# Performance work log

Measured on AMD Instinct MI355X. Metric: run time of the kernel, lower is better.

The kernel has to match this reference:

```python
import jax, jax.numpy as jnp
import numpy as np

NUM_HEADS = 16
QKV_FEATURES = 2048
HEAD_DIM = QKV_FEATURES // NUM_HEADS
THETA = 10000.0


def compute_freqs_cis(dim, length, start_pos=0, theta=THETA, dtype=jnp.float32):
    freqs = 1.0 / theta ** (jnp.arange(0, dim, 2, dtype=jnp.float32) / dim)
    t = jnp.arange(length, dtype=jnp.float32) + start_pos
    freqs = jnp.outer(t, freqs)  # (L, dim//2)
    return jnp.sin(freqs).astype(dtype), jnp.cos(freqs).astype(dtype)


def apply_rotary_emb(x, sin, cos):
    # x: (B, L, H, D); sin/cos: (L, D//2); interleaved-pair rotation
    x1 = x[..., 0::2]
    x2 = x[..., 1::2]
    sin = sin[None, :, None, :]
    cos = cos[None, :, None, :]
    y1 = x1 * cos - x2 * sin
    y2 = x1 * sin + x2 * cos
    return jnp.stack([y1, y2], axis=-1).reshape(x.shape)


def setup_inputs() -> dict:
    key = jax.random.key(0)
    ks = jax.random.split(key, 6)
    B, L, E = 2, 2048, 2048
    s_in = 1.0 / np.sqrt(E)
    s_out = 1.0 / np.sqrt(QKV_FEATURES)
    return {
        "x": jax.random.normal(ks[0], (B, L, E), jnp.float32),
        "Wq": jax.random.normal(ks[1], (E, QKV_FEATURES), jnp.float32) * s_in,
        "Wk": jax.random.normal(ks[2], (E, QKV_FEATURES), jnp.float32) * s_in,
        "Wv": jax.random.normal(ks[3], (E, QKV_FEATURES), jnp.float32) * s_in,
        "Wo": jax.random.normal(ks[4], (QKV_FEATURES, E), jnp.float32) * s_out,
        "bo": jnp.zeros((E,), jnp.float32),
    }


def reference(x, Wq, Wk, Wv, Wo, bo):
    B, L, E = x.shape
    H, D = NUM_HEADS, HEAD_DIM

    q = (x @ Wq).reshape(B, L, H, D)
    k = (x @ Wk).reshape(B, L, H, D)
    v = (x @ Wv).reshape(B, L, H, D)

    sin, cos = compute_freqs_cis(D, L)
    q = apply_rotary_emb(q, sin, cos)
    k = apply_rotary_emb(k, sin, cos)

    scale = D ** (-0.5)
    sim = jnp.einsum("bqhd,bkhd->bhqk", q, k) * scale

    pos = jnp.arange(L)
    causal_mask = pos[None, :] <= pos[:, None]  # (Lq, Lk)
    sim = jnp.where(causal_mask[None, None, :, :], sim, -1e9)

    attn = jax.nn.softmax(sim, axis=-1)
    out = jnp.einsum("bhqk,bkhd->bqhd", attn, v).reshape(B, L, H * D)
    return out @ Wo + bo
```

## Files before the change

### kernel.cpp

```cpp
#include <hip/hip_runtime.h>
#include <hip/hip_bf16.h>
#include <stdint.h>
#include <stddef.h>

#define B_   2
#define L_   2048
#define E_   2048
#define H_   16
#define D_   128
#define F_   2048
#define NROW (B_*L_)
#define QS   6144

typedef __bf16 bf16_t;
typedef __bf16 bf16x4 __attribute__((ext_vector_type(4)));
typedef __bf16 bf16x8 __attribute__((ext_vector_type(8)));
typedef float  f32x4  __attribute__((ext_vector_type(4)));

__device__ __forceinline__ void gload16(const void* g, void* l) {
  __builtin_amdgcn_global_load_lds(
      (const __attribute__((address_space(1))) void*)g,
      (__attribute__((address_space(3))) void*)l, 16, 0, 0);
}

#define VMC(n)  asm volatile("s_waitcnt vmcnt(" #n ")" ::: "memory")
#define BAR_MID do { asm volatile("" ::: "memory"); __builtin_amdgcn_s_barrier(); \
  asm volatile("s_waitcnt lgkmcnt(0)" ::: "memory"); __builtin_amdgcn_sched_barrier(0); } while(0)
#define BAR_END do { asm volatile("" ::: "memory"); __builtin_amdgcn_s_barrier(); } while(0)

__global__ __launch_bounds__(256) void k_prep(const float* __restrict__ x,
                                              const float* __restrict__ Wq,
                                              const float* __restrict__ Wk,
                                              const float* __restrict__ Wv,
                                              const float* __restrict__ Wo,
                                              bf16_t* __restrict__ xb,
                                              bf16_t* __restrict__ wqkvt,
                                              bf16_t* __restrict__ wot,
                                              float2* __restrict__ sc) {
  const int bb = blockIdx.x;
  if (bb < 8192) {
    int i = bb*256 + threadIdx.x;
    float4 v = ((const float4*)x)[i];
    bf16x4 t;
    t[0] = (__bf16)v.x; t[1] = (__bf16)v.y; t[2] = (__bf16)v.z; t[3] = (__bf16)v.w;
    ((bf16x4*)xb)[i] = t;
  } else if (bb < 24576) {
    __shared__ float tile[32][33];
    const int r4 = bb - 8192;
    const int z  = r4 >> 12;
    const int xy = r4 & 4095;
    const int ct = xy & 63, rt = xy >> 6;
    const float* in = (z == 0) ? Wq : (z == 1) ? Wk : (z == 2) ? Wv : Wo;
    bf16_t* out = (z < 3) ? wqkvt + (size_t)z*F_*E_ : wot;
    const int c = threadIdx.x & 31, r0 = threadIdx.x >> 5;
    #pragma unroll
    for (int k = 0; k < 4; k++) {
      int r = r0 + k*8;
      tile[r][c] = in[(size_t)(rt*32 + r)*2048 + ct*32 + c];
    }
    __syncthreads();
    #pragma unroll
    for (int k = 0; k < 4; k++) {
      int r = r0 + k*8;
      out[(size_t)(ct*32 + r)*2048 + rt*32 + c] = (__bf16)tile[c][r];
    }
  } else {
    int id = (bb - 24576)*256 + threadIdx.x;
    int t = id >> 6, i = id & 63;
    float freq = powf(10000.0f, -(float)i / 64.0f);
    float a = (float)t * freq;
    sc[id] = make_float2(cosf(a), sinf(a));
  }
}

__global__ __launch_bounds__(256) void k_ropetv(bf16_t* __restrict__ qkv,
                                                bf16_t* __restrict__ vt,
                                                const float2* __restrict__ sc,
                                                float qscale) {
  const int bb = blockIdx.x;
  if (bb < 16384) {
    const int half = NROW*F_/4;
    int i = bb*256 + threadIdx.x;
    const int part = (i >= half);
    int j = part ? i - half : i;
    int e  = j << 2;
    int d  = e & (F_-1);
    int ii = (d & (D_-1)) >> 1;
    int r  = e >> 11;
    int t  = r & (L_-1);
    bf16_t* p = qkv + (size_t)r*QS + part*F_ + d;
    const float scale = part ? 1.0f : qscale;
    bf16x4 v = *(const bf16x4*)p;
    float2 cs0 = sc[t*64 + ii];
    float2 cs1 = sc[t*64 + ii + 1];
    cs0.x *= scale; cs0.y *= scale; cs1.x *= scale; cs1.y *= scale;
    float x0 = (float)v[0], x1 = (float)v[1], x2 = (float)v[2], x3 = (float)v[3];
    bf16x4 o;
    o[0] = (__bf16)(x0*cs0.x - x1*cs0.y);
    o[1] = (__bf16)(x0*cs0.y + x1*cs0.x);
    o[2] = (__bf16)(x2*cs1.x - x3*cs1.y);
    o[3] = (__bf16)(x2*cs1.y + x3*cs1.x);
    *(bf16x4*)p = o;
  } else {
    __shared__ bf16_t tile[32][33];
    const int r8 = bb - 16384;
    const int lt = r8 & 63, dt = (r8 >> 6) & 3, bh = r8 >> 8;
    const int b = bh >> 4, h = bh & 15;
    const int c = threadIdx.x & 31, r0 = threadIdx.x >> 5;
    #pragma unroll
    for (int k = 0; k < 4; k++) {
      int r = r0 + k*8;
      tile[r][c] = qkv[(size_t)(b*L_ + lt*32 + r)*QS + 2*F_ + h*D_ + dt*32 + c];
    }
    __syncthreads();
    #pragma unroll
    for (int k = 0; k < 4; k++) {
      int r = r0 + k*8;
      vt[(size_t)(bh*D_ + dt*32 + r)*L_ + lt*32 + c] = tile[c][r];
    }
  }
}

#define RDA03(BASE) do { _Pragma("unroll") for (int m_=0;m_<4;m_++) { \
  a[m_][0] = *(const bf16x8*)((BASE) + m_*2048 + cs0); \
  a[m_][1] = *(const bf16x8*)((BASE) + m_*2048 + cs1); } } while(0)
#define RDA47(BASE) do { _Pragma("unroll") for (int m_=0;m_<4;m_++) { \
  a[m_][0] = *(const bf16x8*)((BASE) + (m_+4)*2048 + cs0); \
  a[m_][1] = *(const bf16x8*)((BASE) + (m_+4)*2048 + cs1); } } while(0)
#define RDB01(BASE) do { _Pragma("unroll") for (int n_=0;n_<2;n_++) { \
  b[n_][0] = *(const bf16x8*)((BASE) + n_*2048 + cs0); \
  b[n_][1] = *(const bf16x8*)((BASE) + n_*2048 + cs1); } } while(0)
#define RDB23(BASE) do { _Pragma("unroll") for (int n_=0;n_<2;n_++) { \
  b[2+n_][0] = *(const bf16x8*)((BASE) + (2+n_)*2048 + cs0); \
  b[2+n_][1] = *(const bf16x8*)((BASE) + (2+n_)*2048 + cs1); } } while(0)
#define MM16(MB, NB) do { __builtin_amdgcn_s_setprio(1); \
  _Pragma("unroll") for (int m_=0;m_<4;m_++) { \
    _Pragma("unroll") for (int n_=0;n_<2;n_++) { \
      acc[(MB)+m_][(NB)+n_] = __builtin_amdgcn_mfma_f32_16x16x32_bf16(a[m_][0], b[(NB)+n_][0], acc[(MB)+m_][(NB)+n_], 0, 0, 0); \
      acc[(MB)+m_][(NB)+n_] = __builtin_amdgcn_mfma_f32_16x16x32_bf16(a[m_][1], b[(NB)+n_][1], acc[(MB)+m_][(NB)+n_], 0, 0, 0); } } \
  __builtin_amdgcn_s_setprio(0); } while(0)

template<typename OutT, bool BIAS>
__global__ __launch_bounds__(512, 1) void k_gemm256(const bf16_t* __restrict__ A,
                                                    const bf16_t* __restrict__ BT,
                                                    OutT* __restrict__ C,
                                                    const float* __restrict__ bias,
                                                    int M, int N, int K) {
  __shared__ char sm[131072];
  const int tid = threadIdx.x, lane = tid & 63, wave = tid >> 6;
  const int wr = wave >> 2, wc = wave & 3;
  const int lr = lane & 15, lg = lane >> 4;
  const int nbx = N >> 8;
  const int band = nbx >> 3;
  const int bid = blockIdx.x;
  const int idx = bid >> 3;
  const int bx = (bid & 7)*band + idx % band;
  const int by = idx / band;
  const int row0 = by << 8, col0 = bx << 8;
  const int sr  = tid >> 3;
  const int sxe = ((tid & 7) ^ (sr & 7)) << 3;
  const bf16_t* Ag = A  + (size_t)(row0 + sr)*K + sxe;
  const bf16_t* Bg = BT + (size_t)(col0 + sr)*K + sxe;
  char* smA = sm;
  char* smB = sm + 65536;
  const int dst0 = wave*1024;
  auto stA = [&](int buf, int h, int kt) {
    const bf16_t* s = Ag + (size_t)(h*128)*K + kt;
    char* d = smA + buf*32768 + h*16384 + dst0;
    gload16(s, d); gload16(s + (size_t)64*K, d + 8192);
  };
  auto stB = [&](int buf, int h, int kt) {
    const bf16_t* s = Bg + (size_t)(h*128)*K + kt;
    char* d = smB + buf*32768 + h*16384 + dst0;
    gload16(s, d); gload16(s + (size_t)64*K, d + 8192);
  };
  const int cs0 = (lg ^ (lr & 7)) << 4;
  const int cs1 = ((4 + lg) ^ (lr & 7)) << 4;

  f32x4 acc[8][4] = {};
  bf16x8 a[4][2], b[4][2];

  stA(0,0,0); stA(0,1,0); stB(0,0,0); stB(0,1,0);
  stA(1,0,64); stB(1,0,64); stB(1,1,64);
  VMC(6);
  BAR_END;

  const int nt = K >> 6;
  for (int u = 0; u < nt; u++) {
    const int buf = u & 1;
    const char* Ab = smA + buf*32768 + wr*16384 + lr*128;
    const char* Bb = smB + buf*32768 + (wc >> 1)*16384 + ((wc & 1)*64 + lr)*128;
    RDA03(Ab); RDB01(Bb);
    if (u + 1 < nt) stA(buf^1, 1, (u+1) << 6);
    BAR_MID; MM16(0,0); BAR_END;
    RDB23(Bb);
    BAR_MID; MM16(0,2); BAR_END;
    RDA47(Ab);
    if (u + 2 < nt) { stB(buf, 0, (u+2) << 6); stB(buf, 1, (u+2) << 6); }
    BAR_MID; MM16(4,0); BAR_END;
    if (u + 2 < nt) {
      stA(buf, 0, (u+2) << 6);
      BAR_MID; MM16(4,2); VMC(6); BAR_END;
    } else {
      BAR_MID; MM16(4,2); VMC(0); BAR_END;
    }
  }
  #pragma unroll
  for (int m = 0; m < 8; m++) {
    #pragma unroll
    for (int n = 0; n < 4; n++) {
      const int col = col0 + wc*64 + n*16 + lr;
      const float bv = BIAS ? bias[col] : 0.0f;
      #pragma unroll
      for (int j = 0; j < 4; j++) {
        const int row = row0 + wr*128 + m*16 + lg*4 + j;
        C[(size_t)row*N + col] = (OutT)(acc[m][n][j] + bv);
      }
    }
  }
}

template<typename OutT, bool BIAS>
__global__ __launch_bounds__(256, 3) void k_gemm_bt(const bf16_t* __restrict__ A,
                                                    const bf16_t* __restrict__ BT,
                                                    OutT* __restrict__ C,
                                                    const float* __restrict__ bias,
                                                    int M, int N, int K) {
  __shared__ char sm[49152];
  const int tid = threadIdx.x, lane = tid & 63, wave = tid >> 6;
  const int wr = wave >> 1, wc = wave & 1;
  const int lr = lane & 15, lg = lane >> 4;
  const int nbx = N >> 7;
  const int band = nbx >> 3;
  const int bid = blockIdx.x;
  const int idx = bid >> 3;
  const int bx = (bid & 7)*band + idx % band;
  const int by = idx / band;
  const int row0 = by << 7, col0 = bx << 7;
  const int sr  = tid >> 2;
  const int sxe = (((tid & 3) ^ ((sr >> 1) & 3)) << 3);
  const bf16_t* Ag = A  + (size_t)(row0 + sr)*K + sxe;
  const bf16_t* Bg = BT + (size_t)(col0 + sr)*K + sxe;
  const int dst0 = wave*1024;
  auto stage = [&](int t) {
    char* base = sm + (t % 3)*16384;
    const bf16_t* a = Ag + t*32;
    const bf16_t* b = Bg + t*32;
    gload16(a,                base + dst0);
    gload16(a + (size_t)64*K, base + 4096  + dst0);
    gload16(b,                base + 8192  + dst0);
    gload16(b + (size_t)64*K, base + 12288 + dst0);
  };
  const int cs   = (lg ^ ((lr >> 1) & 3)) << 4;
  const int arow = (wr*64 + lr)*64;
  const int brow = 8192 + (wc*64 + lr)*64;
  f32x4 acc[4][4] = {};
  stage(0); stage(1);
  const int nt = K >> 5;
  for (int t = 0; t < nt; t++) {
    if (t + 2 < nt)      { stage(t + 2); VMC(8); }
    else if (t + 1 < nt) { VMC(4); }
    else                 { VMC(0); }
    __builtin_amdgcn_s_barrier();
    const char* base = sm + (t % 3)*16384;
    bf16x8 af[4], bb[4];
    #pragma unroll
    for (int m = 0; m < 4; m++) af[m] = *(const bf16x8*)(base + arow + m*1024 + cs);
    #pragma unroll
    for (int n = 0; n < 4; n++) bb[n] = *(const bf16x8*)(base + brow + n*1024 + cs);
    asm volatile("s_waitcnt lgkmcnt(0)" ::: "memory");
    __builtin_amdgcn_sched_barrier(0);
    __builtin_amdgcn_s_setprio(1);
    #pragma unroll
    for (int m = 0; m < 4; m++)
      #pragma unroll
      for (int n = 0; n < 4; n++)
        acc[m][n] = __builtin_amdgcn_mfma_f32_16x16x32_bf16(af[m], bb[n], acc[m][n], 0, 0, 0);
    __builtin_amdgcn_s_setprio(0);
    __builtin_amdgcn_s_barrier();
  }
  #pragma unroll
  for (int m = 0; m < 4; m++) {
    #pragma unroll
    for (int n = 0; n < 4; n++) {
      const int col = col0 + wc*64 + n*16 + lr;
      const float bv = BIAS ? bias[col] : 0.0f;
      #pragma unroll
      for (int j = 0; j < 4; j++) {
        const int row = row0 + wr*64 + m*16 + lg*4 + j;
        C[(size_t)row*N + col] = (OutT)(acc[m][n][j] + bv);
      }
    }
  }
}

template<bool MASK>
__device__ __forceinline__ void attn_tile(
    int kv0, int wq0, int lr, int lg,
    const char* __restrict__ Kb, const char* __restrict__ Vb, char* __restrict__ Pb,
    const bf16x8 (&aq)[4], f32x4 (&o)[8], float& mrow, float& lsum) {
  const int swz = (lr & 7) << 4;
  f32x4 s[4] = {};
  #pragma unroll
  for (int kd = 0; kd < 4; kd++) {
    bf16x8 ak[4];
    #pragma unroll
    for (int n = 0; n < 4; n++)
      ak[n] = *(const bf16x8*)(Kb + (n*16 + lr)*256 + (((kd*4 + lg) << 4) ^ swz));
    __builtin_amdgcn_s_setprio(1);
    #pragma unroll
    for (int n = 0; n < 4; n++)
      s[n] = __builtin_amdgcn_mfma_f32_16x16x32_bf16(ak[n], aq[kd], s[n], 0, 0, 0);
    __builtin_amdgcn_s_setprio(0);
  }
  if (MASK) {
    const int q = wq0 + lr;
    #pragma unroll
    for (int n = 0; n < 4; n++)
      #pragma unroll
      for (int j = 0; j < 4; j++)
        if (kv0 + n*16 + lg*4 + j > q) s[n][j] = -30000.0f;
  }
  float pmax = fmaxf(
      fmaxf(fmaxf(fmaxf(s[0][0], s[0][1]), fmaxf(s[0][2], s[0][3])),
            fmaxf(fmaxf(s[1][0], s[1][1]), fmaxf(s[1][2], s[1][3]))),
      fmaxf(fmaxf(fmaxf(s[2][0], s[2][1]), fmaxf(s[2][2], s[2][3])),
            fmaxf(fmaxf(s[3][0], s[3][1]), fmaxf(s[3][2], s[3][3]))));
  pmax = fmaxf(pmax, __shfl_xor(pmax, 16));
  pmax = fmaxf(pmax, __shfl_xor(pmax, 32));
  if (!__all(pmax - mrow <= 8.0f)) {
    const float mnew = fmaxf(mrow, pmax);
    const float corr = exp2f(mrow - mnew);
    mrow = mnew;
    lsum *= corr;
    #pragma unroll
    for (int n2 = 0; n2 < 8; n2++) o[n2] *= corr;
  }
  float rs = 0.0f;
  #pragma unroll
  for (int n = 0; n < 4; n++)
    #pragma unroll
    for (int j = 0; j < 4; j++) {
      float p = exp2f(s[n][j] - mrow);
      s[n][j] = p;
      rs += p;
    }
  rs += __shfl_xor(rs, 16);
  rs += __shfl_xor(rs, 32);
  lsum += rs;
  #pragma unroll
  for (int n = 0; n < 4; n++) {
    bf16x4 pw;
    pw[0] = (__bf16)s[n][0]; pw[1] = (__bf16)s[n][1];
    pw[2] = (__bf16)s[n][2]; pw[3] = (__bf16)s[n][3];
    *(bf16x4*)(Pb + ((lr*128 + n*32 + lg*8) ^ swz)) = pw;
  }
  #pragma unroll
  for (int ks = 0; ks < 2; ks++) {
    bf16x8 pb = *(const bf16x8*)(Pb + ((lr*128 + ks*64 + lg*16) ^ swz));
    __builtin_amdgcn_s_setprio(1);
    #pragma unroll
    for (int n2 = 0; n2 < 8; n2++) {
      bf16x8 av = *(const bf16x8*)(Vb + (n2*16 + lr)*128 + (((ks*4 + lg) << 4) ^ swz));
      o[n2] = __builtin_amdgcn_mfma_f32_16x16x32_bf16(av, pb, o[n2], 0, 0, 0);
    }
    __builtin_amdgcn_s_setprio(0);
  }
}

__global__ __launch_bounds__(512, 4) void k_attn(const bf16_t* __restrict__ QKV,
                                                 const bf16_t* __restrict__ Vt,
                                                 bf16_t* __restrict__ O) {
  __shared__ bf16_t Ks[2][64*128];
  __shared__ bf16_t Vs[2][128*64];
  __shared__ bf16_t Pl[8][16*64];
  const int tid = threadIdx.x, lane = tid & 63, wave = tid >> 6;
  const int bidx = blockIdx.x;
  const int xcd = bidx & 7, idx = bidx >> 3;
  const int bh  = xcd*4 + (idx & 3);
  const int qt  = 15 - (idx >> 2);
  const int b = bh >> 4, h = bh & 15;
  const int wq0 = qt*128 + wave*16;
  const int lr = lane & 15, lg = lane >> 4;
  char* Pb = (char*)&Pl[wave][0];
  const bf16_t* Q = QKV;
  const bf16_t* K = QKV + F_;

  bf16x8 aq[4];
  #pragma unroll
  for (int kd = 0; kd < 4; kd++)
    aq[kd] = *(const bf16x8*)&Q[(size_t)(b*L_ + wq0 + lr)*QS + h*D_ + kd*32 + lg*8];

  const int kr = tid >> 4, kc = tid & 15;
  const bf16_t* Kg0 = K + (size_t)(b*L_ + kr)*QS + h*D_ + ((kc ^ (kr & 7)) << 3);
  const int vr = tid >> 3, vc = tid & 7;
  const bf16_t* Vg0 = Vt + (size_t)((b*H_ + h)*D_ + vr)*L_ + ((vc ^ (vr & 7)) << 3);

  f32x4 o[8] = {};
  float mrow = -3.0e38f, lsum = 0.0f;
  const int ntb   = 2*qt + 2;
  const int nfull = (wq0 + 1) >> 6;
  const int nmine = ((wq0 + 15) >> 6) + 1;

  {
    char* kb = (char*)&Ks[0][0] + wave*1024;
    char* vb = (char*)&Vs[0][0] + wave*1024;
    gload16(Kg0,                 kb);
    gload16(Kg0 + (size_t)32*QS, kb + 8192);
    gload16(Vg0,                 vb);
    gload16(Vg0 + (size_t)64*L_, vb + 8192);
  }
  __syncthreads();

  int buf = 0;
  for (int t = 0; t < ntb; t++) {
    if (t + 1 < ntb) {
      const int kn = (t+1)*64;
      char* kb = (char*)&Ks[buf^1][0] + wave*1024;
      char* vb = (char*)&Vs[buf^1][0] + wave*1024;
      const bf16_t* kg = Kg0 + (size_t)kn*QS;
      const bf16_t* vg = Vg0 + kn;
      gload16(kg,                 kb);
      gload16(kg + (size_t)32*QS, kb + 8192);
      gload16(vg,                 vb);
      gload16(vg + (size_t)64*L_, vb + 8192);
    }
    const char* Kb = (const char*)&Ks[buf][0];
    const char* Vb = (const char*)&Vs[buf][0];
    if (t < nfull)
      attn_tile<false>(t*64, wq0, lr, lg, Kb, Vb, Pb, aq, o, mrow, lsum);
    else if (t < nmine)
      attn_tile<true >(t*64, wq0, lr, lg, Kb, Vb, Pb, aq, o, mrow, lsum);
    __syncthreads();
    buf ^= 1;
  }
  const float inv = 1.0f / lsum;
  bf16_t* orow = O + (size_t)(b*L_ + wq0 + lr)*F_ + h*D_ + lg*4;
  #pragma unroll
  for (int n2 = 0; n2 < 8; n2++) {
    bf16x4 ov;
    ov[0] = (__bf16)(o[n2][0]*inv); ov[1] = (__bf16)(o[n2][1]*inv);
    ov[2] = (__bf16)(o[n2][2]*inv); ov[3] = (__bf16)(o[n2][3]*inv);
    *(bf16x4*)(orow + n2*16) = ov;
  }
}

extern "C" void kernel_launch(void* const* d_in, const int* in_sizes, int n_in,
                              void* d_out, int out_size, void* d_ws, size_t ws_size,
                              hipStream_t stream) {
  const float* x  = (const float*)d_in[0];
  const float* Wq = (const float*)d_in[1];
  const float* Wk = (const float*)d_in[2];
  const float* Wv = (const float*)d_in[3];
  const float* Wo = (const float*)d_in[4];
  const float* bo = (const float*)d_in[5];
  float* out = (float*)d_out;

  char* ws = (char*)d_ws;
  size_t off = 0;
  auto alloc = [&](size_t bytes) {
    char* p = ws + off;
    off = (off + bytes + 255) & ~(size_t)255;
    return p;
  };
  bf16_t* xb    = (bf16_t*)alloc((size_t)NROW*E_*2);
  bf16_t* wqkvt = (bf16_t*)alloc((size_t)3*F_*E_*2);
  bf16_t* wot   = (bf16_t*)alloc((size_t)F_*E_*2);
  float2* sc    = (float2*)alloc((size_t)L_*64*sizeof(float2));
  bf16_t* qkv   = (bf16_t*)alloc((size_t)NROW*QS*2);
  bf16_t* vt    = (bf16_t*)alloc((size_t)NROW*F_*2);
  bf16_t* ob    = xb;

  const float scale2 = 0.08838834764831845f * 1.44269504088896f;

  k_prep<<<dim3(25088), 256, 0, stream>>>(x, Wq, Wk, Wv, Wo, xb, wqkvt, wot, sc);

  k_gemm256<bf16_t, false><<<dim3((QS/256)*(NROW/256)), 512, 0, stream>>>(
      xb, wqkvt, qkv, nullptr, NROW, QS, E_);

  k_ropetv<<<dim3(24576), 256, 0, stream>>>(qkv, vt, sc, scale2);

  k_attn<<<dim3(512), 512, 0, stream>>>(qkv, vt, ob);

  k_gemm_bt<float, true><<<dim3((E_/128)*(NROW/128)), 256, 0, stream>>>(
      ob, wot, out, bo, NROW, E_, F_);
}
```

Baseline: 402.2 us.

## Fuse RoPE into QKV GEMM epilogue and unify GEMMs on a 128x256 triple-buffered kernel

Moves the rotary embedding and Q scaling into the QKV GEMM epilogue, using a lane shuffle to fetch the paired element, so the separate in-place RoPE pass over Q and K is removed. The V transpose becomes its own smaller kernel. The 256x256 double-buffered GEMM is reshaped to 128x256 tiles with a three-stage LDS ring, and the output projection now uses this kernel in place of the 128x128 one. This trades fewer accumulators per block and more blocks for a longer epilogue and higher LDS use per block.

```diff
diff --git a/kernel.cpp b/kernel.cpp
--- a/kernel.cpp
+++ b/kernel.cpp
@@ -73,80 +73,48 @@
   }
 }
 
-__global__ __launch_bounds__(256) void k_ropetv(bf16_t* __restrict__ qkv,
-                                                bf16_t* __restrict__ vt,
-                                                const float2* __restrict__ sc,
-                                                float qscale) {
+__global__ __launch_bounds__(256) void k_vt(const bf16_t* __restrict__ qkv,
+                                            bf16_t* __restrict__ vt) {
+  __shared__ bf16_t tile[32][33];
   const int bb = blockIdx.x;
-  if (bb < 16384) {
-    const int half = NROW*F_/4;
-    int i = bb*256 + threadIdx.x;
-    const int part = (i >= half);
-    int j = part ? i - half : i;
-    int e  = j << 2;
-    int d  = e & (F_-1);
-    int ii = (d & (D_-1)) >> 1;
-    int r  = e >> 11;
-    int t  = r & (L_-1);
-    bf16_t* p = qkv + (size_t)r*QS + part*F_ + d;
-    const float scale = part ? 1.0f : qscale;
-    bf16x4 v = *(const bf16x4*)p;
-    float2 cs0 = sc[t*64 + ii];
-    float2 cs1 = sc[t*64 + ii + 1];
-    cs0.x *= scale; cs0.y *= scale; cs1.x *= scale; cs1.y *= scale;
-    float x0 = (float)v[0], x1 = (float)v[1], x2 = (float)v[2], x3 = (float)v[3];
-    bf16x4 o;
-    o[0] = (__bf16)(x0*cs0.x - x1*cs0.y);
-    o[1] = (__bf16)(x0*cs0.y + x1*cs0.x);
-    o[2] = (__bf16)(x2*cs1.x - x3*cs1.y);
-    o[3] = (__bf16)(x2*cs1.y + x3*cs1.x);
-    *(bf16x4*)p = o;
-  } else {
-    __shared__ bf16_t tile[32][33];
-    const int r8 = bb - 16384;
-    const int lt = r8 & 63, dt = (r8 >> 6) & 3, bh = r8 >> 8;
-    const int b = bh >> 4, h = bh & 15;
-    const int c = threadIdx.x & 31, r0 = threadIdx.x >> 5;
-    #pragma unroll
-    for (int k = 0; k < 4; k++) {
-      int r = r0 + k*8;
-      tile[r][c] = qkv[(size_t)(b*L_ + lt*32 + r)*QS + 2*F_ + h*D_ + dt*32 + c];
-    }
-    __syncthreads();
-    #pragma unroll
-    for (int k = 0; k < 4; k++) {
-      int r = r0 + k*8;
-      vt[(size_t)(bh*D_ + dt*32 + r)*L_ + lt*32 + c] = tile[c][r];
-    }
-  }
-}
-
-#define RDA03(BASE) do { _Pragma("unroll") for (int m_=0;m_<4;m_++) { \
+  const int lt = bb & 63, dt = (bb >> 6) & 3, bh = bb >> 8;
+  const int b = bh >> 4, h = bh & 15;
+  const int c = threadIdx.x & 31, r0 = threadIdx.x >> 5;
+  #pragma unroll
+  for (int k = 0; k < 4; k++) {
+    int r = r0 + k*8;
+    tile[r][c] = qkv[(size_t)(b*L_ + lt*32 + r)*QS + 2*F_ + h*D_ + dt*32 + c];
+  }
+  __syncthreads();
+  #pragma unroll
+  for (int k = 0; k < 4; k++) {
+    int r = r0 + k*8;
+    vt[(size_t)(bh*D_ + dt*32 + r)*L_ + lt*32 + c] = tile[c][r];
+  }
+}
+
+#define RDA(BASE) do { _Pragma("unroll") for (int m_=0;m_<4;m_++) { \
   a[m_][0] = *(const bf16x8*)((BASE) + m_*2048 + cs0); \
   a[m_][1] = *(const bf16x8*)((BASE) + m_*2048 + cs1); } } while(0)
-#define RDA47(BASE) do { _Pragma("unroll") for (int m_=0;m_<4;m_++) { \
-  a[m_][0] = *(const bf16x8*)((BASE) + (m_+4)*2048 + cs0); \
-  a[m_][1] = *(const bf16x8*)((BASE) + (m_+4)*2048 + cs1); } } while(0)
-#define RDB01(BASE) do { _Pragma("unroll") for (int n_=0;n_<2;n_++) { \
-  b[n_][0] = *(const bf16x8*)((BASE) + n_*2048 + cs0); \
-  b[n_][1] = *(const bf16x8*)((BASE) + n_*2048 + cs1); } } while(0)
-#define RDB23(BASE) do { _Pragma("unroll") for (int n_=0;n_<2;n_++) { \
-  b[2+n_][0] = *(const bf16x8*)((BASE) + (2+n_)*2048 + cs0); \
-  b[2+n_][1] = *(const bf16x8*)((BASE) + (2+n_)*2048 + cs1); } } while(0)
-#define MM16(MB, NB) do { __builtin_amdgcn_s_setprio(1); \
+#define RDB(BASE, NB) do { _Pragma("unroll") for (int n_=0;n_<2;n_++) { \
+  bb_[n_][0] = *(const bf16x8*)((BASE) + ((NB)+n_)*2048 + cs0); \
+  bb_[n_][1] = *(const bf16x8*)((BASE) + ((NB)+n_)*2048 + cs1); } } while(0)
+#define MMQ(NB) do { __builtin_amdgcn_s_setprio(1); \
   _Pragma("unroll") for (int m_=0;m_<4;m_++) { \
     _Pragma("unroll") for (int n_=0;n_<2;n_++) { \
-      acc[(MB)+m_][(NB)+n_] = __builtin_amdgcn_mfma_f32_16x16x32_bf16(a[m_][0], b[(NB)+n_][0], acc[(MB)+m_][(NB)+n_], 0, 0, 0); \
-      acc[(MB)+m_][(NB)+n_] = __builtin_amdgcn_mfma_f32_16x16x32_bf16(a[m_][1], b[(NB)+n_][1], acc[(MB)+m_][(NB)+n_], 0, 0, 0); } } \
+      acc[m_][(NB)+n_] = __builtin_amdgcn_mfma_f32_16x16x32_bf16(a[m_][0], bb_[n_][0], acc[m_][(NB)+n_], 0, 0, 0); \
+      acc[m_][(NB)+n_] = __builtin_amdgcn_mfma_f32_16x16x32_bf16(a[m_][1], bb_[n_][1], acc[m_][(NB)+n_], 0, 0, 0); } } \
   __builtin_amdgcn_s_setprio(0); } while(0)
 
-template<typename OutT, bool BIAS>
+template<typename OutT, int MODE>
 __global__ __launch_bounds__(512, 1) void k_gemm256(const bf16_t* __restrict__ A,
                                                     const bf16_t* __restrict__ BT,
                                                     OutT* __restrict__ C,
                                                     const float* __restrict__ bias,
+                                                    const float2* __restrict__ sc,
+                                                    float qscale,
                                                     int M, int N, int K) {
-  __shared__ char sm[131072];
+  __shared__ char sm[147456];
   const int tid = threadIdx.x, lane = tid & 63, wave = tid >> 6;
   const int wr = wave >> 2, wc = wave & 3;
   const int lr = lane & 15, lg = lane >> 4;
@@ -156,139 +124,88 @@
   const int idx = bid >> 3;
   const int bx = (bid & 7)*band + idx % band;
   const int by = idx / band;
-  const int row0 = by << 8, col0 = bx << 8;
+  const int row0 = by << 7, col0 = bx << 8;
   const int sr  = tid >> 3;
   const int sxe = ((tid & 7) ^ (sr & 7)) << 3;
   const bf16_t* Ag = A  + (size_t)(row0 + sr)*K + sxe;
   const bf16_t* Bg = BT + (size_t)(col0 + sr)*K + sxe;
-  char* smA = sm;
-  char* smB = sm + 65536;
-  const int dst0 = wave*1024;
-  auto stA = [&](int buf, int h, int kt) {
-    const bf16_t* s = Ag + (size_t)(h*128)*K + kt;
-    char* d = smA + buf*32768 + h*16384 + dst0;
+  auto stA = [&](int t) {
+    const bf16_t* s = Ag + t*64;
+    char* d = sm + (t % 3)*16384 + wave*1024;
     gload16(s, d); gload16(s + (size_t)64*K, d + 8192);
   };
-  auto stB = [&](int buf, int h, int kt) {
-    const bf16_t* s = Bg + (size_t)(h*128)*K + kt;
-    char* d = smB + buf*32768 + h*16384 + dst0;
+  auto stB01 = [&](int t) {
+    const bf16_t* s = Bg + t*64;
+    char* d = sm + 49152 + (t % 3)*32768 + wave*1024;
+    gload16(s, d); gload16(s + (size_t)64*K, d + 8192);
+  };
+  auto stB23 = [&](int t) {
+    const bf16_t* s = Bg + (size_t)128*K + t*64;
+    char* d = sm + 49152 + (t % 3)*32768 + 16384 + wave*1024;
     gload16(s, d); gload16(s + (size_t)64*K, d + 8192);
   };
   const int cs0 = (lg ^ (lr & 7)) << 4;
   const int cs1 = ((4 + lg) ^ (lr & 7)) << 4;
 
-  f32x4 acc[8][4] = {};
-  bf16x8 a[4][2], b[4][2];
-
-  stA(0,0,0); stA(0,1,0); stB(0,0,0); stB(0,1,0);
-  stA(1,0,64); stB(1,0,64); stB(1,1,64);
+  f32x4 acc[4][4] = {};
+  bf16x8 a[4][2], bb_[2][2];
+
+  stA(0); stB01(0); stB23(0);
+  stA(1); stB01(1); stB23(1);
   VMC(6);
   BAR_END;
 
   const int nt = K >> 6;
   for (int u = 0; u < nt; u++) {
-    const int buf = u & 1;
-    const char* Ab = smA + buf*32768 + wr*16384 + lr*128;
-    const char* Bb = smB + buf*32768 + (wc >> 1)*16384 + ((wc & 1)*64 + lr)*128;
-    RDA03(Ab); RDB01(Bb);
-    if (u + 1 < nt) stA(buf^1, 1, (u+1) << 6);
-    BAR_MID; MM16(0,0); BAR_END;
-    RDB23(Bb);
-    BAR_MID; MM16(0,2); BAR_END;
-    RDA47(Ab);
-    if (u + 2 < nt) { stB(buf, 0, (u+2) << 6); stB(buf, 1, (u+2) << 6); }
-    BAR_MID; MM16(4,0); BAR_END;
-    if (u + 2 < nt) {
-      stA(buf, 0, (u+2) << 6);
-      BAR_MID; MM16(4,2); VMC(6); BAR_END;
-    } else {
-      BAR_MID; MM16(4,2); VMC(0); BAR_END;
-    }
-  }
-  #pragma unroll
-  for (int m = 0; m < 8; m++) {
+    const int bi = u % 3;
+    const char* Ab = sm + bi*16384 + (wr*64 + lr)*128;
+    const char* Bb = sm + 49152 + bi*32768 + (wc*64 + lr)*128;
+    RDA(Ab);
+    RDB(Bb, 0);
+    if (u + 2 < nt) { stA(u+2); stB01(u+2); }
+    BAR_MID;
+    MMQ(0);
+    BAR_END;
+    RDB(Bb, 2);
+    if (u + 2 < nt) stB23(u+2);
+    BAR_MID;
+    MMQ(2);
+    if (u + 2 < nt) { VMC(6); } else { VMC(0); }
+    BAR_END;
+  }
+  #pragma unroll
+  for (int m = 0; m < 4; m++) {
     #pragma unroll
     for (int n = 0; n < 4; n++) {
       const int col = col0 + wc*64 + n*16 + lr;
-      const float bv = BIAS ? bias[col] : 0.0f;
-      #pragma unroll
-      for (int j = 0; j < 4; j++) {
-        const int row = row0 + wr*128 + m*16 + lg*4 + j;
-        C[(size_t)row*N + col] = (OutT)(acc[m][n][j] + bv);
-      }
-    }
-  }
-}
-
-template<typename OutT, bool BIAS>
-__global__ __launch_bounds__(256, 3) void k_gemm_bt(const bf16_t* __restrict__ A,
-                                                    const bf16_t* __restrict__ BT,
-                                                    OutT* __restrict__ C,
-                                                    const float* __restrict__ bias,
-                                                    int M, int N, int K) {
-  __shared__ char sm[49152];
-  const int tid = threadIdx.x, lane = tid & 63, wave = tid >> 6;
-  const int wr = wave >> 1, wc = wave & 1;
-  const int lr = lane & 15, lg = lane >> 4;
-  const int nbx = N >> 7;
-  const int band = nbx >> 3;
-  const int bid = blockIdx.x;
-  const int idx = bid >> 3;
-  const int bx = (bid & 7)*band + idx % band;
-  const int by = idx / band;
-  const int row0 = by << 7, col0 = bx << 7;
-  const int sr  = tid >> 2;
-  const int sxe = (((tid & 3) ^ ((sr >> 1) & 3)) << 3);
-  const bf16_t* Ag = A  + (size_t)(row0 + sr)*K + sxe;
-  const bf16_t* Bg = BT + (size_t)(col0 + sr)*K + sxe;
-  const int dst0 = wave*1024;
-  auto stage = [&](int t) {
-    char* base = sm + (t % 3)*16384;
-    const bf16_t* a = Ag + t*32;
-    const bf16_t* b = Bg + t*32;
-    gload16(a,                base + dst0);
-    gload16(a + (size_t)64*K, base + 4096  + dst0);
-    gload16(b,                base + 8192  + dst0);
-    gload16(b + (size_t)64*K, base + 12288 + dst0);
-  };
-  const int cs   = (lg ^ ((lr >> 1) & 3)) << 4;
-  const int arow = (wr*64 + lr)*64;
-  const int brow = 8192 + (wc*64 + lr)*64;
-  f32x4 acc[4][4] = {};
-  stage(0); stage(1);
-  const int nt = K >> 5;
-  for (int t = 0; t < nt; t++) {
-    if (t + 2 < nt)      { stage(t + 2); VMC(8); }
-    else if (t + 1 < nt) { VMC(4); }
-    else                 { VMC(0); }
-    __builtin_amdgcn_s_barrier();
-    const char* base = sm + (t % 3)*16384;
-    bf16x8 af[4], bb[4];
-    #pragma unroll
-    for (int m = 0; m < 4; m++) af[m] = *(const bf16x8*)(base + arow + m*1024 + cs);
-    #pragma unroll
-    for (int n = 0; n < 4; n++) bb[n] = *(const bf16x8*)(base + brow + n*1024 + cs);
-    asm volatile("s_waitcnt lgkmcnt(0)" ::: "memory");
-    __builtin_amdgcn_sched_barrier(0);
-    __builtin_amdgcn_s_setprio(1);
-    #pragma unroll
-    for (int m = 0; m < 4; m++)
-      #pragma unroll
-      for (int n = 0; n < 4; n++)
-        acc[m][n] = __builtin_amdgcn_mfma_f32_16x16x32_bf16(af[m], bb[n], acc[m][n], 0, 0, 0);
-    __builtin_amdgcn_s_setprio(0);
-    __builtin_amdgcn_s_barrier();
-  }
-  #pragma unroll
-  for (int m = 0; m < 4; m++) {
-    #pragma unroll
-    for (int n = 0; n < 4; n++) {
-      const int col = col0 + wc*64 + n*16 + lr;
-      const float bv = BIAS ? bias[col] : 0.0f;
-      #pragma unroll
-      for (int j = 0; j < 4; j++) {
-        const int row = row0 + wr*64 + m*16 + lg*4 + j;
-        C[(size_t)row*N + col] = (OutT)(acc[m][n][j] + bv);
+      if (MODE == 2) {
+        const float bv = bias[col];
+        #pragma unroll
+        for (int j = 0; j < 4; j++) {
+          const int row = row0 + wr*64 + m*16 + lg*4 + j;
+          C[(size_t)row*N + col] = (OutT)(acc[m][n][j] + bv);
+        }
+      } else {
+        const int third = col >> 11;
+        const int ii    = (col & (D_-1)) >> 1;
+        const bool odd  = (lr & 1);
+        const float ss  = (third == 0) ? qscale : 1.0f;
+        #pragma unroll
+        for (int j = 0; j < 4; j++) {
+          const int row = row0 + wr*64 + m*16 + lg*4 + j;
+          const float v0 = acc[m][n][j];
+          const float vp = __shfl_xor(v0, 1);
+          float res;
+          if (third == 2) {
+            res = v0;
+          } else {
+            const int t = row & (L_-1);
+            const float2 cs = sc[t*64 + ii];
+            const float cosv = cs.x * ss, sinv = cs.y * ss;
+            res = odd ? (vp*sinv + v0*cosv) : (v0*cosv - vp*sinv);
+          }
+          C[(size_t)row*N + col] = (OutT)res;
+        }
       }
     }
   }
@@ -475,13 +392,13 @@
 
   k_prep<<<dim3(25088), 256, 0, stream>>>(x, Wq, Wk, Wv, Wo, xb, wqkvt, wot, sc);
 
-  k_gemm256<bf16_t, false><<<dim3((QS/256)*(NROW/256)), 512, 0, stream>>>(
-      xb, wqkvt, qkv, nullptr, NROW, QS, E_);
-
-  k_ropetv<<<dim3(24576), 256, 0, stream>>>(qkv, vt, sc, scale2);
+  k_gemm256<bf16_t, 1><<<dim3((QS/256)*(NROW/128)), 512, 0, stream>>>(
+      xb, wqkvt, qkv, nullptr, sc, scale2, NROW, QS, E_);
+
+  k_vt<<<dim3(8192), 256, 0, stream>>>(qkv, vt);
 
   k_attn<<<dim3(512), 512, 0, stream>>>(qkv, vt, ob);
 
-  k_gemm_bt<float, true><<<dim3((E_/128)*(NROW/128)), 256, 0, stream>>>(
-      ob, wot, out, bo, NROW, E_, F_);
-}
+  k_gemm256<float, 2><<<dim3((E_/256)*(NROW/128)), 512, 0, stream>>>(
+      ob, wot, out, bo, nullptr, 1.0f, NROW, E_, F_);
+}
```

Measured after the change: 423.2 us. 5.2% more time.
